# Optimization experiments

Hardware: AMD Instinct MI355X
Metric: run time of the kernel (lower is better)

The kernel has to match this reference:

```python
import jax, jax.numpy as jnp
import numpy as np

N_HEADS = 32
N_KV_HEADS = 8
HEAD_DIM = 128
N_QUERY = N_HEADS // N_KV_HEADS  # 4
ROPE_BASE = 10000.0


def _rope_tables(seq_len, head_dim):
    # inv freqs over pairs of channels (Llama-style interleaved complex rotation)
    inv_freq = 1.0 / (ROPE_BASE ** (jnp.arange(0, head_dim, 2, dtype=jnp.float32) / head_dim))
    t = jnp.arange(seq_len, dtype=jnp.float32)
    ang = t[:, None] * inv_freq[None, :]           # [s, d/2]
    return jnp.cos(ang)[None, :, None, :], jnp.sin(ang)[None, :, None, :]  # [1,s,1,d/2]


def _apply_rope(x, cos, sin):
    # x: [b, s, h, d]; consecutive channel pairs are (real, imag)
    xr = x[..., 0::2]
    xi = x[..., 1::2]
    out_r = xr * cos - xi * sin
    out_i = xr * sin + xi * cos
    return jnp.stack([out_r, out_i], axis=-1).reshape(x.shape)


def setup_inputs() -> dict:
    key = jax.random.key(0)
    kx, kq, kk, kv, ko = jax.random.split(key, 5)
    dim = 4096
    kv_dim = N_KV_HEADS * HEAD_DIM
    scale = 0.02
    return {
        "x": jax.random.normal(kx, (2, 2048, dim), dtype=jnp.float32),
        "wq": jax.random.normal(kq, (dim, dim), dtype=jnp.float32) * scale,
        "wk": jax.random.normal(kk, (dim, kv_dim), dtype=jnp.float32) * scale,
        "wv": jax.random.normal(kv, (dim, kv_dim), dtype=jnp.float32) * scale,
        "wo": jax.random.normal(ko, (dim, dim), dtype=jnp.float32) * scale,
    }


def reference(x, wq, wk, wv, wo):
    b, s, _ = x.shape
    xq = (x @ wq).reshape(b, s, N_HEADS, HEAD_DIM)
    xk = (x @ wk).reshape(b, s, N_KV_HEADS, HEAD_DIM)
    xv = (x @ wv).reshape(b, s, N_KV_HEADS, HEAD_DIM)

    cos, sin = _rope_tables(s, HEAD_DIM)
    xq = _apply_rope(xq, cos, sin)
    xk = _apply_rope(xk, cos, sin)

    # GQA without materializing the KV expand: group query heads per kv head.
    qh = xq.reshape(b, s, N_KV_HEADS, N_QUERY, HEAD_DIM)
    scores = jnp.einsum('bsgnd,btgd->bgnst', qh, xk) / jnp.sqrt(
        jnp.asarray(HEAD_DIM, dtype=xq.dtype))  # [b,g,n,s,t]

    # causal mask: -inf above diagonal
    causal = jnp.arange(s)[:, None] >= jnp.arange(s)[None, :]
    scores = jnp.where(causal[None, None, None, :, :], scores, -jnp.inf)

    att = jax.nn.softmax(scores.astype(jnp.float32), axis=-1).astype(xq.dtype)
    out = jnp.einsum('bgnst,btgd->bsgnd', att, xv).reshape(b, s, N_HEADS * HEAD_DIM)
    return out @ wo
```

## Files before the change

### kernel.cpp

```cpp
#include <hip/hip_runtime.h>
#include <hip/hip_bf16.h>

typedef __attribute__((ext_vector_type(8))) short short8;
typedef __attribute__((ext_vector_type(4))) float f32x4;
typedef __attribute__((ext_vector_type(16))) float f32x16;

#define GLD16(gp, lp) __builtin_amdgcn_global_load_lds( \
    (const __attribute__((address_space(1))) unsigned int*)(gp), \
    (__attribute__((address_space(3))) unsigned int*)(lp), 16, 0, 0)

static __device__ __forceinline__ float bf2f(unsigned short u) {
    union { unsigned int i; float f; } v; v.i = ((unsigned int)u) << 16; return v.f;
}
static __device__ __forceinline__ short f2bf(float f) {
    union { float f; unsigned int i; } v; v.f = f;
    unsigned int r = v.i + 0x7FFFu + ((v.i >> 16) & 1u);
    return (short)(r >> 16);
}
static __device__ __forceinline__ unsigned int pack2bf(float lo, float hi) {
    return ((unsigned int)(unsigned short)f2bf(hi) << 16) | (unsigned int)(unsigned short)f2bf(lo);
}
static __device__ __forceinline__ unsigned int cvtpk(float lo, float hi) {
    unsigned int w;
    asm("v_cvt_pk_bf16_f32 %0, %1, %2" : "=v"(w) : "v"(lo), "v"(hi));
    return w;
}

__global__ void cast_f32_bf16(const float* __restrict__ src, short* __restrict__ dst, int n) {
    int i = (blockIdx.x * 256 + threadIdx.x) * 4;
    if (i >= n) return;
    float4 v = *(const float4*)(src + i);
    short4 o;
    o.x = f2bf(v.x); o.y = f2bf(v.y); o.z = f2bf(v.z); o.w = f2bf(v.w);
    *(short4*)(dst + i) = o;
}

__global__ void transpose_cast(const float* __restrict__ src, short* __restrict__ dst,
                               int N, int dstStride) {
    __shared__ float tile[32][33];
    int k0 = blockIdx.x * 32, n0 = blockIdx.y * 32;
    int t = threadIdx.x, c = t & 31, r = t >> 5;
#pragma unroll
    for (int p = 0; p < 4; ++p)
        tile[r + p * 8][c] = src[(size_t)(k0 + r + p * 8) * N + n0 + c];
    __syncthreads();
#pragma unroll
    for (int p = 0; p < 4; ++p)
        dst[(size_t)(n0 + r + p * 8) * dstStride + k0 + c] = f2bf(tile[c][r + p * 8]);
}

__global__ void transpose_v(const short* __restrict__ qkv, short* __restrict__ vt) {
    __shared__ short tile[32][33];
    int s0 = blockIdx.x * 32, d0 = blockIdx.y * 32;
    int bh = blockIdx.z;
    int b = bh >> 3, h = bh & 7;
    const short* src = qkv + (size_t)b * 2048 * 6144 + 5120 + h * 128;
    short* dst = vt + (size_t)bh * 128 * 2048;
    int t = threadIdx.x, c = t & 31, r = t >> 5;
#pragma unroll
    for (int p = 0; p < 4; ++p)
        tile[r + p * 8][c] = src[(size_t)(s0 + r + p * 8) * 6144 + d0 + c];
    __syncthreads();
#pragma unroll
    for (int p = 0; p < 4; ++p)
        dst[(size_t)(d0 + r + p * 8) * 2048 + s0 + c] = tile[c][r + p * 8];
}

__global__ void rope_tables(float* __restrict__ cs) {
    int i = blockIdx.x * 256 + threadIdx.x;
    int s = i >> 6, d2 = i & 63;
    float inv = expf(-9.210340371976184f * (float)(2 * d2) * (1.0f / 128.0f));
    float ang = (float)s * inv;
    float sn, c;
    sincosf(ang, &sn, &c);
    cs[(size_t)i * 2] = c;
    cs[(size_t)i * 2 + 1] = sn;
}

template<int NH>
__global__ void rope_apply(const short* __restrict__ qkv, const float* __restrict__ cs,
                           short* __restrict__ dst, int colOff, float scale) {
    int i = blockIdx.x * 256 + threadIdx.x;
    int d2 = i & 63;
    int t2 = i >> 6;
    int h = t2 % NH;
    int bs = t2 / NH;
    int s = bs & 2047;
    int b = bs >> 11;
    unsigned int pr = *(const unsigned int*)(qkv + (size_t)bs * 6144 + colOff + h * 128 + 2 * d2);
    float xr = bf2f((unsigned short)(pr & 0xFFFFu));
    float xi = bf2f((unsigned short)(pr >> 16));
    const float* cp = cs + ((size_t)s * 64 + d2) * 2;
    float c = cp[0], sn = cp[1];
    float outr = (xr * c - xi * sn) * scale;
    float outi = (xr * sn + xi * c) * scale;
    *(unsigned int*)(dst + ((size_t)(b * NH + h) * 2048 + s) * 128 + 2 * d2) = pack2bf(outr, outi);
}

template<bool BF16OUT>
__global__ __launch_bounds__(256, 2) void gemm_bt(const short* __restrict__ A,
                                                  const short* __restrict__ Bt,
                                                  void* __restrict__ Cv,
                                                  int N, int K) {
    __shared__ short As[128 * 64];
    __shared__ short Bs[128 * 64];
    const int tid = threadIdx.x;
    const int lane = tid & 63;
    const int wid = tid >> 6;
    const int lr = lane & 15;
    const int lq = lane >> 4;
    const int m0 = blockIdx.x * 128;
    const int n0 = blockIdx.y * 128;
    const int wr = (wid >> 1) * 64;
    const int wc = (wid & 1) * 64;
    f32x4 acc[4][4];
#pragma unroll
    for (int i = 0; i < 4; ++i)
#pragma unroll
        for (int j = 0; j < 4; ++j) acc[i][j] = f32x4{0.f, 0.f, 0.f, 0.f};

    const short* aBase = A + (size_t)m0 * K;
    const short* bBase = Bt + (size_t)n0 * K;

    for (int k0 = 0; k0 < K; k0 += 64) {
#pragma unroll
        for (int j = 0; j < 4; ++j) {
            int c = (wid * 4 + j) * 64 + lane;
            int row = c >> 3;
            int cb = ((c & 7) << 4) ^ ((row & 7) << 4);
            GLD16(aBase + (size_t)row * K + k0 + (cb >> 1), As + (wid * 4 + j) * 512);
            GLD16(bBase + (size_t)row * K + k0 + (cb >> 1), Bs + (wid * 4 + j) * 512);
        }
        __syncthreads();
#pragma unroll
        for (int ks = 0; ks < 2; ++ks) {
            short8 af[4], bfr[4];
#pragma unroll
            for (int mi = 0; mi < 4; ++mi) {
                int row = wr + mi * 16 + lr;
                int cb = (ks * 64 + lq * 16) ^ ((row & 7) << 4);
                af[mi] = *(const short8*)(As + row * 64 + (cb >> 1));
            }
#pragma unroll
            for (int ni = 0; ni < 4; ++ni) {
                int row = wc + ni * 16 + lr;
                int cb = (ks * 64 + lq * 16) ^ ((row & 7) << 4);
                bfr[ni] = *(const short8*)(Bs + row * 64 + (cb >> 1));
            }
#pragma unroll
            for (int mi = 0; mi < 4; ++mi)
#pragma unroll
                for (int ni = 0; ni < 4; ++ni)
                    acc[mi][ni] = __builtin_amdgcn_mfma_f32_16x16x32_bf16(af[mi], bfr[ni], acc[mi][ni], 0, 0, 0);
        }
        __syncthreads();
    }
#pragma unroll
    for (int mi = 0; mi < 4; ++mi)
#pragma unroll
        for (int ni = 0; ni < 4; ++ni)
#pragma unroll
            for (int r = 0; r < 4; ++r) {
                int row = m0 + wr + mi * 16 + lq * 4 + r;
                int col = n0 + wc + ni * 16 + lr;
                float v = acc[mi][ni][r];
                if constexpr (BF16OUT) ((short*)Cv)[(size_t)row * N + col] = f2bf(v);
                else                   ((float*)Cv)[(size_t)row * N + col] = v;
            }
}

__global__ __launch_bounds__(256, 2) void attn_kernel(const short* __restrict__ Qr,
                                                      const short* __restrict__ Kr,
                                                      const short* __restrict__ Vt,
                                                      short* __restrict__ Out) {
    __shared__ short Ks[64 * 128];
    __shared__ short Vs[128 * 64];
    const int qb = 15 - blockIdx.x;
    const int bh = blockIdx.y;
    const int b = bh >> 5;
    const int qh = bh & 31;
    const int kvh = qh >> 2;
    const int tid = threadIdx.x;
    const int lane = tid & 63;
    const int w = tid >> 6;
    const int l31 = lane & 31;
    const int hi = lane >> 5;
    const int qg0 = qb * 128 + w * 32;

    const short* qbase = Qr + ((size_t)bh * 2048 + qg0 + l31) * 128 + hi * 8;
    short8 qf[8];
#pragma unroll
    for (int ks = 0; ks < 8; ++ks)
        qf[ks] = *(const short8*)(qbase + ks * 16);

    const short* kbase = Kr + (size_t)(b * 8 + kvh) * 2048 * 128;
    const short* vbase = Vt + (size_t)(b * 8 + kvh) * 128 * 2048;

    float m_run = -INFINITY, l_run = 0.0f;
    f32x16 oacc[4];
#pragma unroll
    for (int dt = 0; dt < 4; ++dt) oacc[dt] = f32x16{0,0,0,0,0,0,0,0,0,0,0,0,0,0,0,0};

    const int nkb = 2 * qb + 2;
    for (int kb = 0; kb < nkb; ++kb) {
        const int s0 = kb * 64;
#pragma unroll
        for (int j = 0; j < 4; ++j) {
            int c = j * 256 + tid;
            int krow = c >> 4;
            int kcol = ((c & 15) ^ (krow & 7)) * 8;
            GLD16(kbase + (size_t)(s0 + krow) * 128 + kcol, Ks + (size_t)c * 8);
            int vrow = c >> 3;
            int vcol = ((c & 7) ^ (vrow & 7)) * 8;
            GLD16(vbase + (size_t)vrow * 2048 + s0 + vcol, Vs + (size_t)c * 8);
        }
        __syncthreads();

        if (s0 <= qg0 + 31) {
            f32x16 st0 = f32x16{0,0,0,0,0,0,0,0,0,0,0,0,0,0,0,0};
            f32x16 st1 = f32x16{0,0,0,0,0,0,0,0,0,0,0,0,0,0,0,0};
            __builtin_amdgcn_s_setprio(1);
#pragma unroll
            for (int ks = 0; ks < 8; ++ks) {
                int row0 = l31;
                int ch0 = ((2 * ks + hi) ^ (row0 & 7)) * 8;
                short8 kf0 = *(const short8*)(Ks + row0 * 128 + ch0);
                st0 = __builtin_amdgcn_mfma_f32_32x32x16_bf16(kf0, qf[ks], st0, 0, 0, 0);
                int row1 = 32 + l31;
                int ch1 = ((2 * ks + hi) ^ (row1 & 7)) * 8;
                short8 kf1 = *(const short8*)(Ks + row1 * 128 + ch1);
                st1 = __builtin_amdgcn_mfma_f32_32x32x16_bf16(kf1, qf[ks], st1, 0, 0, 0);
            }
            __builtin_amdgcn_s_setprio(0);

            const int q = qg0 + l31;
            if (s0 + 63 > qg0) {
#pragma unroll
                for (int i = 0; i < 16; ++i) {
                    int kvr = (i & 3) + 8 * (i >> 2) + 4 * hi;
                    if (s0 + kvr > q)      st0[i] = -INFINITY;
                    if (s0 + 32 + kvr > q) st1[i] = -INFINITY;
                }
            }

            float mx = -INFINITY;
#pragma unroll
            for (int i = 0; i < 16; ++i) mx = fmaxf(mx, fmaxf(st0[i], st1[i]));
            mx = fmaxf(mx, __shfl_xor(mx, 32, 64));

            const bool defer = __all(mx - m_run <= 8.0f);
            float mN, alpha;
            if (defer) { mN = m_run; alpha = 1.0f; }
            else       { mN = fmaxf(m_run, mx); alpha = __expf(m_run - mN); }

            float p0[16], p1[16];
            float rsum = 0.0f;
#pragma unroll
            for (int i = 0; i < 16; ++i) {
                p0[i] = __expf(st0[i] - mN);
                p1[i] = __expf(st1[i] - mN);
                rsum += p0[i] + p1[i];
            }
            rsum += __shfl_xor(rsum, 32, 64);
            l_run = l_run * alpha + rsum;
            m_run = mN;
            if (!defer) {
#pragma unroll
                for (int dt = 0; dt < 4; ++dt)
#pragma unroll
                    for (int i = 0; i < 16; ++i) oacc[dt][i] *= alpha;
            }

            short8 pfr[4];
#pragma unroll
            for (int kvs = 0; kvs < 4; ++kvs) {
                const float* pp = (kvs < 2) ? p0 : p1;
                const int h8 = (kvs & 1) * 8;
                unsigned int x0 = cvtpk(pp[h8 + 0], pp[h8 + 1]);
                unsigned int x1 = cvtpk(pp[h8 + 2], pp[h8 + 3]);
                unsigned int y0 = cvtpk(pp[h8 + 4], pp[h8 + 5]);
                unsigned int y1 = cvtpk(pp[h8 + 6], pp[h8 + 7]);
                asm("v_permlane32_swap_b32 %0, %1" : "+v"(x0), "+v"(y0));
                asm("v_permlane32_swap_b32 %0, %1" : "+v"(x1), "+v"(y1));
                union { unsigned int u[4]; short8 s; } uu;
                uu.u[0] = x0; uu.u[1] = x1; uu.u[2] = y0; uu.u[3] = y1;
                pfr[kvs] = uu.s;
            }

            __builtin_amdgcn_s_setprio(1);
#pragma unroll
            for (int dt = 0; dt < 4; ++dt) {
                int row = dt * 32 + l31;
#pragma unroll
                for (int kvs = 0; kvs < 4; ++kvs) {
                    int ch = ((2 * kvs + hi) ^ (row & 7)) * 8;
                    short8 vf = *(const short8*)(Vs + row * 64 + ch);
                    oacc[dt] = __builtin_amdgcn_mfma_f32_32x32x16_bf16(vf, pfr[kvs], oacc[dt], 0, 0, 0);
                }
            }
            __builtin_amdgcn_s_setprio(0);
        }
        __syncthreads();
    }

    const float inv = 1.0f / l_run;
    const size_t row = (size_t)b * 2048 + qg0 + l31;
    short* obase = Out + row * 4096 + qh * 128;
#pragma unroll
    for (int dt = 0; dt < 4; ++dt) {
#pragma unroll
        for (int g = 0; g < 4; ++g) {
            short4 o4;
            o4.x = f2bf(oacc[dt][g * 4 + 0] * inv);
            o4.y = f2bf(oacc[dt][g * 4 + 1] * inv);
            o4.z = f2bf(oacc[dt][g * 4 + 2] * inv);
            o4.w = f2bf(oacc[dt][g * 4 + 3] * inv);
            *(short4*)(obase + dt * 32 + g * 8 + hi * 4) = o4;
        }
    }
}


extern "C" void kernel_launch(void* const* d_in, const int* in_sizes, int n_in,
                              void* d_out, int out_size, void* d_ws, size_t ws_size,
                              hipStream_t stream) {
    const float* x  = (const float*)d_in[0];
    const float* wq = (const float*)d_in[1];
    const float* wk = (const float*)d_in[2];
    const float* wv = (const float*)d_in[3];
    const float* wo = (const float*)d_in[4];
    float* out = (float*)d_out;
    char* ws = (char*)d_ws;

    short* wt_qkv = (short*)(ws + 0);
    short* xb     = (short*)(ws + 50331648);
    short* qkv    = (short*)(ws + 83886080);
    short* wt_o   = (short*)(ws + 83886080);
    short* qr     = (short*)(ws + 134217728);
    short* kr     = (short*)(ws + 167772160);
    short* vt     = (short*)(ws + 176160768);
    float* tab    = (float*)(ws + 184549376);

    cast_f32_bf16<<<16384, 256, 0, stream>>>(x, xb, 16777216);
    transpose_cast<<<dim3(128, 128), 256, 0, stream>>>(wq, wt_qkv, 4096, 4096);
    transpose_cast<<<dim3(128, 32),  256, 0, stream>>>(wk, wt_qkv + (size_t)4096 * 4096, 1024, 4096);
    transpose_cast<<<dim3(128, 32),  256, 0, stream>>>(wv, wt_qkv + (size_t)5120 * 4096, 1024, 4096);
    rope_tables<<<512, 256, 0, stream>>>(tab);
    gemm_bt<true><<<dim3(32, 48), 256, 0, stream>>>(xb, wt_qkv, (void*)qkv, 6144, 4096);
    rope_apply<32><<<32768, 256, 0, stream>>>(qkv, tab, qr, 0, 0.08838834764831845f);
    rope_apply<8><<<8192, 256, 0, stream>>>(qkv, tab, kr, 4096, 1.0f);
    transpose_v<<<dim3(64, 4, 16), 256, 0, stream>>>(qkv, vt);
    transpose_cast<<<dim3(128, 128), 256, 0, stream>>>(wo, wt_o, 4096, 4096);
    attn_kernel<<<dim3(16, 64), 256, 0, stream>>>(qr, kr, vt, xb);
    gemm_bt<false><<<dim3(32, 32), 256, 0, stream>>>(xb, wt_o, (void*)out, 4096, 4096);
}
```

Measured before the change: 597.3 us.

## Replace GEMM with 256x256-tile, 4-stage pipelined 32x32 MFMA kernel

Rewrites the projection GEMM to use 256x256 output tiles with 512 threads and a 4-deep LDS ring buffer filled by async global-to-LDS loads. Uses fine-grained vmcnt waits, one barrier per k-step and an XCD-aware block remap. Switches from 16x16x32 to 32x32x16 MFMA and raises priority during the MFMA block. The aim is more operand reuse, latency hiding and L2 locality. In exchange it needs 128KB of dynamic LDS, which limits occupancy, and gives fewer blocks per GEMM (384 and 256), a possible tail-imbalance risk.

```diff
diff --git a/kernel.cpp b/kernel.cpp
--- a/kernel.cpp
+++ b/kernel.cpp
@@ -98,72 +98,114 @@
 }
 
 template<bool BF16OUT>
-__global__ __launch_bounds__(256, 2) void gemm_bt(const short* __restrict__ A,
+__global__ __launch_bounds__(512, 2) void gemm256(const short* __restrict__ A,
                                                   const short* __restrict__ Bt,
                                                   void* __restrict__ Cv,
-                                                  int N, int K) {
-    __shared__ short As[128 * 64];
-    __shared__ short Bs[128 * 64];
+                                                  int Mtiles, int N, int K) {
+    extern __shared__ __align__(16) short lds[];
+    short* As = lds;
+    short* Bs = lds + 32768;
     const int tid = threadIdx.x;
     const int lane = tid & 63;
     const int wid = tid >> 6;
-    const int lr = lane & 15;
-    const int lq = lane >> 4;
-    const int m0 = blockIdx.x * 128;
-    const int n0 = blockIdx.y * 128;
-    const int wr = (wid >> 1) * 64;
-    const int wc = (wid & 1) * 64;
-    f32x4 acc[4][4];
-#pragma unroll
-    for (int i = 0; i < 4; ++i)
-#pragma unroll
-        for (int j = 0; j < 4; ++j) acc[i][j] = f32x4{0.f, 0.f, 0.f, 0.f};
+    const int l31 = lane & 31;
+    const int hi = lane >> 5;
+    const int wr = wid >> 2;
+    const int wc = wid & 3;
+
+    const int nwg = gridDim.x;
+    const int id = blockIdx.x;
+    const int sid = (id & 7) * (nwg >> 3) + (id >> 3);
+    const int m0 = (sid % Mtiles) * 256;
+    const int n0 = (sid / Mtiles) * 256;
 
     const short* aBase = A + (size_t)m0 * K;
     const short* bBase = Bt + (size_t)n0 * K;
-
-    for (int k0 = 0; k0 < K; k0 += 64) {
-#pragma unroll
-        for (int j = 0; j < 4; ++j) {
-            int c = (wid * 4 + j) * 64 + lane;
-            int row = c >> 3;
-            int cb = ((c & 7) << 4) ^ ((row & 7) << 4);
-            GLD16(aBase + (size_t)row * K + k0 + (cb >> 1), As + (wid * 4 + j) * 512);
-            GLD16(bBase + (size_t)row * K + k0 + (cb >> 1), Bs + (wid * 4 + j) * 512);
-        }
-        __syncthreads();
-#pragma unroll
-        for (int ks = 0; ks < 2; ++ks) {
-            short8 af[4], bfr[4];
-#pragma unroll
-            for (int mi = 0; mi < 4; ++mi) {
-                int row = wr + mi * 16 + lr;
-                int cb = (ks * 64 + lq * 16) ^ ((row & 7) << 4);
-                af[mi] = *(const short8*)(As + row * 64 + (cb >> 1));
-            }
-#pragma unroll
-            for (int ni = 0; ni < 4; ++ni) {
-                int row = wc + ni * 16 + lr;
-                int cb = (ks * 64 + lq * 16) ^ ((row & 7) << 4);
-                bfr[ni] = *(const short8*)(Bs + row * 64 + (cb >> 1));
-            }
+    const int NT = K >> 5;
+
+    auto stage = [&](int t) {
+        const int buf = t & 3;
+        const short* as = aBase + t * 32;
+        const short* bs = bBase + t * 32;
+#pragma unroll
+        for (int j = 0; j < 2; ++j) {
+            int c = j * 512 + tid;
+            int row = c >> 2;
+            int sc = ((c & 3) ^ (row & 3)) * 8;
+            GLD16(as + (size_t)row * K + sc, As + buf * 8192 + c * 8);
+        }
+#pragma unroll
+        for (int j = 0; j < 2; ++j) {
+            int c = j * 512 + tid;
+            int row = c >> 2;
+            int sc = ((c & 3) ^ (row & 3)) * 8;
+            GLD16(bs + (size_t)row * K + sc, Bs + buf * 8192 + c * 8);
+        }
+    };
+
+    f32x16 acc[4][2];
+#pragma unroll
+    for (int mi = 0; mi < 4; ++mi)
+#pragma unroll
+        for (int ni = 0; ni < 2; ++ni)
+            acc[mi][ni] = f32x16{0,0,0,0,0,0,0,0,0,0,0,0,0,0,0,0};
+
+    stage(0); stage(1); stage(2);
+    asm volatile("s_waitcnt vmcnt(8)" ::: "memory");
+    __builtin_amdgcn_sched_barrier(0);
+    __builtin_amdgcn_s_barrier();
+    __builtin_amdgcn_sched_barrier(0);
+
+    for (int t = 0; t < NT; ++t) {
+        const int buf = t & 3;
+        if (t + 3 < NT) stage(t + 3);
+
+        short8 af[4][2], bfr[2][2];
+#pragma unroll
+        for (int mi = 0; mi < 4; ++mi) {
+            int row = wr * 128 + mi * 32 + l31;
+#pragma unroll
+            for (int ks = 0; ks < 2; ++ks)
+                af[mi][ks] = *(const short8*)(As + buf * 8192 + (row * 4 + ((ks * 2 + hi) ^ (row & 3))) * 8);
+        }
+#pragma unroll
+        for (int ni = 0; ni < 2; ++ni) {
+            int row = wc * 64 + ni * 32 + l31;
+#pragma unroll
+            for (int ks = 0; ks < 2; ++ks)
+                bfr[ni][ks] = *(const short8*)(Bs + buf * 8192 + (row * 4 + ((ks * 2 + hi) ^ (row & 3))) * 8);
+        }
+
+        __builtin_amdgcn_s_setprio(1);
+#pragma unroll
+        for (int ks = 0; ks < 2; ++ks)
 #pragma unroll
             for (int mi = 0; mi < 4; ++mi)
 #pragma unroll
-                for (int ni = 0; ni < 4; ++ni)
-                    acc[mi][ni] = __builtin_amdgcn_mfma_f32_16x16x32_bf16(af[mi], bfr[ni], acc[mi][ni], 0, 0, 0);
-        }
-        __syncthreads();
+                for (int ni = 0; ni < 2; ++ni)
+                    acc[mi][ni] = __builtin_amdgcn_mfma_f32_32x32x16_bf16(af[mi][ks], bfr[ni][ks], acc[mi][ni], 0, 0, 0);
+        __builtin_amdgcn_s_setprio(0);
+
+        __builtin_amdgcn_sched_barrier(0);
+        if (t + 4 <= NT)      { asm volatile("s_waitcnt vmcnt(8)" ::: "memory"); }
+        else if (t + 3 == NT) { asm volatile("s_waitcnt vmcnt(4)" ::: "memory"); }
+        else if (t + 2 == NT) { asm volatile("s_waitcnt vmcnt(0)" ::: "memory"); }
+        __builtin_amdgcn_sched_barrier(0);
+        if (t + 1 < NT) {
+            __builtin_amdgcn_s_barrier();
+            __builtin_amdgcn_sched_barrier(0);
+        }
     }
+
 #pragma unroll
     for (int mi = 0; mi < 4; ++mi)
 #pragma unroll
-        for (int ni = 0; ni < 4; ++ni)
-#pragma unroll
-            for (int r = 0; r < 4; ++r) {
-                int row = m0 + wr + mi * 16 + lq * 4 + r;
-                int col = n0 + wc + ni * 16 + lr;
-                float v = acc[mi][ni][r];
+        for (int ni = 0; ni < 2; ++ni)
+#pragma unroll
+            for (int i = 0; i < 16; ++i) {
+                int row = m0 + wr * 128 + mi * 32 + (i & 3) + 8 * (i >> 2) + 4 * hi;
+                int col = n0 + wc * 64 + ni * 32 + l31;
+                float v = acc[mi][ni][i];
                 if constexpr (BF16OUT) ((short*)Cv)[(size_t)row * N + col] = f2bf(v);
                 else                   ((float*)Cv)[(size_t)row * N + col] = v;
             }
@@ -346,11 +388,11 @@
     transpose_cast<<<dim3(128, 32),  256, 0, stream>>>(wk, wt_qkv + (size_t)4096 * 4096, 1024, 4096);
     transpose_cast<<<dim3(128, 32),  256, 0, stream>>>(wv, wt_qkv + (size_t)5120 * 4096, 1024, 4096);
     rope_tables<<<512, 256, 0, stream>>>(tab);
-    gemm_bt<true><<<dim3(32, 48), 256, 0, stream>>>(xb, wt_qkv, (void*)qkv, 6144, 4096);
+    gemm256<true><<<384, 512, 131072, stream>>>(xb, wt_qkv, (void*)qkv, 16, 6144, 4096);
     rope_apply<32><<<32768, 256, 0, stream>>>(qkv, tab, qr, 0, 0.08838834764831845f);
     rope_apply<8><<<8192, 256, 0, stream>>>(qkv, tab, kr, 4096, 1.0f);
     transpose_v<<<dim3(64, 4, 16), 256, 0, stream>>>(qkv, vt);
     transpose_cast<<<dim3(128, 128), 256, 0, stream>>>(wo, wt_o, 4096, 4096);
     attn_kernel<<<dim3(16, 64), 256, 0, stream>>>(qr, kr, vt, xb);
-    gemm_bt<false><<<dim3(32, 32), 256, 0, stream>>>(xb, wt_o, (void*)out, 4096, 4096);
-}
+    gemm256<false><<<256, 512, 131072, stream>>>(xb, wt_o, (void*)out, 16, 4096, 4096);
+}
```

After: 708.5 us. +18.6%, slower.

## Fuse RoPE, head layout and V transpose into QKV GEMM epilogue

Applied to the files above, without the earlier changes.

Replaces the generic QKV GEMM plus separate rope_apply and transpose_v kernels with a dedicated GEMM whose epilogue applies RoPE and scaling to the Q/K accumulators via lane shuffles and writes head-major Q/K and transposed V directly. This removes the intermediate qkv buffer's write and reread and three kernel launches. In exchange, the epilogue does scattered 2-byte stores for Q/K and strided short4 stores for V, which may coalesce poorly.

```diff
diff --git a/kernel.cpp b/kernel.cpp
--- a/kernel.cpp
+++ b/kernel.cpp
@@ -16,9 +16,6 @@
     union { float f; unsigned int i; } v; v.f = f;
     unsigned int r = v.i + 0x7FFFu + ((v.i >> 16) & 1u);
     return (short)(r >> 16);
-}
-static __device__ __forceinline__ unsigned int pack2bf(float lo, float hi) {
-    return ((unsigned int)(unsigned short)f2bf(hi) << 16) | (unsigned int)(unsigned short)f2bf(lo);
 }
 static __device__ __forceinline__ unsigned int cvtpk(float lo, float hi) {
     unsigned int w;
@@ -47,23 +44,6 @@
 #pragma unroll
     for (int p = 0; p < 4; ++p)
         dst[(size_t)(n0 + r + p * 8) * dstStride + k0 + c] = f2bf(tile[c][r + p * 8]);
-}
-
-__global__ void transpose_v(const short* __restrict__ qkv, short* __restrict__ vt) {
-    __shared__ short tile[32][33];
-    int s0 = blockIdx.x * 32, d0 = blockIdx.y * 32;
-    int bh = blockIdx.z;
-    int b = bh >> 3, h = bh & 7;
-    const short* src = qkv + (size_t)b * 2048 * 6144 + 5120 + h * 128;
-    short* dst = vt + (size_t)bh * 128 * 2048;
-    int t = threadIdx.x, c = t & 31, r = t >> 5;
-#pragma unroll
-    for (int p = 0; p < 4; ++p)
-        tile[r + p * 8][c] = src[(size_t)(s0 + r + p * 8) * 6144 + d0 + c];
-    __syncthreads();
-#pragma unroll
-    for (int p = 0; p < 4; ++p)
-        dst[(size_t)(d0 + r + p * 8) * 2048 + s0 + c] = tile[c][r + p * 8];
 }
 
 __global__ void rope_tables(float* __restrict__ cs) {
@@ -77,24 +57,114 @@
     cs[(size_t)i * 2 + 1] = sn;
 }
 
-template<int NH>
-__global__ void rope_apply(const short* __restrict__ qkv, const float* __restrict__ cs,
-                           short* __restrict__ dst, int colOff, float scale) {
-    int i = blockIdx.x * 256 + threadIdx.x;
-    int d2 = i & 63;
-    int t2 = i >> 6;
-    int h = t2 % NH;
-    int bs = t2 / NH;
-    int s = bs & 2047;
-    int b = bs >> 11;
-    unsigned int pr = *(const unsigned int*)(qkv + (size_t)bs * 6144 + colOff + h * 128 + 2 * d2);
-    float xr = bf2f((unsigned short)(pr & 0xFFFFu));
-    float xi = bf2f((unsigned short)(pr >> 16));
-    const float* cp = cs + ((size_t)s * 64 + d2) * 2;
-    float c = cp[0], sn = cp[1];
-    float outr = (xr * c - xi * sn) * scale;
-    float outi = (xr * sn + xi * c) * scale;
-    *(unsigned int*)(dst + ((size_t)(b * NH + h) * 2048 + s) * 128 + 2 * d2) = pack2bf(outr, outi);
+__global__ __launch_bounds__(256, 2) void gemm_qkv(const short* __restrict__ A,
+                                                   const short* __restrict__ Bt,
+                                                   short* __restrict__ Qr,
+                                                   short* __restrict__ Kr,
+                                                   short* __restrict__ Vt,
+                                                   const float* __restrict__ tab) {
+    __shared__ short As[128 * 64];
+    __shared__ short Bs[128 * 64];
+    const int K = 4096;
+    const int tid = threadIdx.x;
+    const int lane = tid & 63;
+    const int wid = tid >> 6;
+    const int lr = lane & 15;
+    const int lq = lane >> 4;
+    const int m0 = blockIdx.x * 128;
+    const int n0 = blockIdx.y * 128;
+    const int wr = (wid >> 1) * 64;
+    const int wc = (wid & 1) * 64;
+    f32x4 acc[4][4];
+#pragma unroll
+    for (int i = 0; i < 4; ++i)
+#pragma unroll
+        for (int j = 0; j < 4; ++j) acc[i][j] = f32x4{0.f, 0.f, 0.f, 0.f};
+
+    const short* aBase = A + (size_t)m0 * K;
+    const short* bBase = Bt + (size_t)n0 * K;
+
+    for (int k0 = 0; k0 < K; k0 += 64) {
+#pragma unroll
+        for (int j = 0; j < 4; ++j) {
+            int c = (wid * 4 + j) * 64 + lane;
+            int row = c >> 3;
+            int cb = ((c & 7) << 4) ^ ((row & 7) << 4);
+            GLD16(aBase + (size_t)row * K + k0 + (cb >> 1), As + (wid * 4 + j) * 512);
+            GLD16(bBase + (size_t)row * K + k0 + (cb >> 1), Bs + (wid * 4 + j) * 512);
+        }
+        __syncthreads();
+#pragma unroll
+        for (int ks = 0; ks < 2; ++ks) {
+            short8 af[4], bfr[4];
+#pragma unroll
+            for (int mi = 0; mi < 4; ++mi) {
+                int row = wr + mi * 16 + lr;
+                int cb = (ks * 64 + lq * 16) ^ ((row & 7) << 4);
+                af[mi] = *(const short8*)(As + row * 64 + (cb >> 1));
+            }
+#pragma unroll
+            for (int ni = 0; ni < 4; ++ni) {
+                int row = wc + ni * 16 + lr;
+                int cb = (ks * 64 + lq * 16) ^ ((row & 7) << 4);
+                bfr[ni] = *(const short8*)(Bs + row * 64 + (cb >> 1));
+            }
+#pragma unroll
+            for (int mi = 0; mi < 4; ++mi)
+#pragma unroll
+                for (int ni = 0; ni < 4; ++ni)
+                    acc[mi][ni] = __builtin_amdgcn_mfma_f32_16x16x32_bf16(af[mi], bfr[ni], acc[mi][ni], 0, 0, 0);
+        }
+        __syncthreads();
+    }
+
+    const float2* t2 = (const float2*)tab;
+    if (n0 < 5120) {
+        const bool isQ = (n0 < 4096);
+        short* dst = isQ ? Qr : Kr;
+        const int nh = isQ ? 32 : 8;
+        const int coff = isQ ? 0 : 4096;
+        const float sc = isQ ? 0.08838834764831845f : 1.0f;
+#pragma unroll
+        for (int mi = 0; mi < 4; ++mi)
+#pragma unroll
+            for (int ni = 0; ni < 4; ++ni) {
+                int col = n0 + wc + ni * 16 + lr - coff;
+                int h = col >> 7;
+                int d = col & 127;
+                int d2 = d >> 1;
+                const bool odd = d & 1;
+#pragma unroll
+                for (int r = 0; r < 4; ++r) {
+                    int row = m0 + wr + mi * 16 + lq * 4 + r;
+                    int s = row & 2047;
+                    int b = row >> 11;
+                    float v = acc[mi][ni][r];
+                    float vp = __shfl_xor(v, 1, 64);
+                    float2 cs2 = t2[s * 64 + d2];
+                    float o = odd ? (v * cs2.x + vp * cs2.y) : (v * cs2.x - vp * cs2.y);
+                    dst[((size_t)(b * nh + h) * 2048 + s) * 128 + d] = f2bf(o * sc);
+                }
+            }
+    } else {
+#pragma unroll
+        for (int mi = 0; mi < 4; ++mi)
+#pragma unroll
+            for (int ni = 0; ni < 4; ++ni) {
+                int col = n0 + wc + ni * 16 + lr - 5120;
+                int h = col >> 7;
+                int d = col & 127;
+                int row0 = m0 + wr + mi * 16 + lq * 4;
+                int s0 = row0 & 2047;
+                int b = row0 >> 11;
+                short4 o4;
+                o4.x = f2bf(acc[mi][ni][0]);
+                o4.y = f2bf(acc[mi][ni][1]);
+                o4.z = f2bf(acc[mi][ni][2]);
+                o4.w = f2bf(acc[mi][ni][3]);
+                *(short4*)(Vt + (size_t)(b * 8 + h) * 128 * 2048 + (size_t)d * 2048 + s0) = o4;
+            }
+    }
 }
 
 template<bool BF16OUT>
@@ -334,7 +404,6 @@
 
     short* wt_qkv = (short*)(ws + 0);
     short* xb     = (short*)(ws + 50331648);
-    short* qkv    = (short*)(ws + 83886080);
     short* wt_o   = (short*)(ws + 83886080);
     short* qr     = (short*)(ws + 134217728);
     short* kr     = (short*)(ws + 167772160);
@@ -346,10 +415,7 @@
     transpose_cast<<<dim3(128, 32),  256, 0, stream>>>(wk, wt_qkv + (size_t)4096 * 4096, 1024, 4096);
     transpose_cast<<<dim3(128, 32),  256, 0, stream>>>(wv, wt_qkv + (size_t)5120 * 4096, 1024, 4096);
     rope_tables<<<512, 256, 0, stream>>>(tab);
-    gemm_bt<true><<<dim3(32, 48), 256, 0, stream>>>(xb, wt_qkv, (void*)qkv, 6144, 4096);
-    rope_apply<32><<<32768, 256, 0, stream>>>(qkv, tab, qr, 0, 0.08838834764831845f);
-    rope_apply<8><<<8192, 256, 0, stream>>>(qkv, tab, kr, 4096, 1.0f);
-    transpose_v<<<dim3(64, 4, 16), 256, 0, stream>>>(qkv, vt);
+    gemm_qkv<<<dim3(32, 48), 256, 0, stream>>>(xb, wt_qkv, qr, kr, vt, tab);
     transpose_cast<<<dim3(128, 128), 256, 0, stream>>>(wo, wt_o, 4096, 4096);
     attn_kernel<<<dim3(16, 64), 256, 0, stream>>>(qr, kr, vt, xb);
     gemm_bt<false><<<dim3(32, 32), 256, 0, stream>>>(xb, wt_o, (void*)out, 4096, 4096);
```

After: 576.6 us. 1.04x faster.
